# Kernel tuning notes

Hardware: AMD Instinct MI355X
Metric: run time of the kernel (lower is better)

## Reference

```python
import jax, jax.numpy as jnp
import numpy as np


def setup_inputs() -> dict:
    key = jax.random.key(0)
    k1, k2 = jax.random.split(key)
    TOKENS, IN, OUT = 32768, 1024, 1024
    x = jax.random.normal(k1, (TOKENS, IN), dtype=jnp.float32)
    # weight init: uniform(-1, 1) over [out_features, in_features]
    weight = jax.random.uniform(k2, (OUT, IN), dtype=jnp.float32, minval=-1.0, maxval=1.0)
    b = jnp.zeros((OUT,), dtype=jnp.float32)
    return {"x": x, "weight": weight, "b": b}


def reference(x, weight, b):
    # ternary quantization: sign() zeros out exact zeros; mask keeps nonzeros
    sign = jnp.sign(weight)
    mask = (weight != 0).astype(x.dtype)
    w_q = sign * mask  # [out, in], values in {-1, 0, 1}
    # F.linear: x @ w_q.T + b
    return jnp.einsum("ti,oi->to", x, w_q) + b
```

## Files before the change

kernel.cpp:

```cpp
#include <hip/hip_runtime.h>
#include <hip/hip_bf16.h>


typedef int   i32x4  __attribute__((ext_vector_type(4)));
typedef int   i32x16 __attribute__((ext_vector_type(16)));
typedef float f32x4  __attribute__((ext_vector_type(4)));

#define BM 128
#define BN 128
#define BK 64

__device__ __forceinline__ void async16(const void* gptr, void* lptr) {
    __builtin_amdgcn_global_load_lds(
        (const __attribute__((address_space(1))) unsigned int*)gptr,
        (__attribute__((address_space(3))) unsigned int*)lptr,
        16, 0, 0);
}

__device__ __forceinline__ int clamp127(int v) {
    v = v > 127 ? 127 : v;
    v = v < -127 ? -127 : v;
    return v;
}

__device__ __forceinline__ int pack4(int a, int b, int c, int d) {
    return (a & 255) | ((b & 255) << 8) | ((c & 255) << 16) | ((d & 255) << 24);
}

__device__ __forceinline__ int sgnb(float v) {
    return (v > 0.0f) ? 1 : ((v < 0.0f) ? -1 : 0);
}


__global__ __launch_bounds__(256)
void quant_pre(const float* __restrict__ x, const float* __restrict__ w,
               signed char* __restrict__ xq, signed char* __restrict__ wq,
               float* __restrict__ scales, int M, int K, long nw, int xblocks) {
    const int tid = threadIdx.x;

    if ((int)blockIdx.x >= xblocks) {
        long i = ((long)(blockIdx.x - xblocks) * 256 + tid) * 8;
        if (i + 8 > nw) return;
        const float4* p = (const float4*)(w + i);
        float4 a = p[0];
        float4 b = p[1];
        int lo = pack4(sgnb(a.x), sgnb(a.y), sgnb(a.z), sgnb(a.w));
        int hi = pack4(sgnb(b.x), sgnb(b.y), sgnb(b.z), sgnb(b.w));
        int2 v; v.x = lo; v.y = hi;
        *(int2*)(wq + i) = v;
        return;
    }

    const int wv   = tid >> 6;
    const int lane = tid & 63;
    const int row  = blockIdx.x * 4 + wv;
    if (row >= M) return;

    const float* xr = x + (long)row * K;
    const int chunks = K >> 8;
    float4 v[8];
    float m = 0.0f;
#pragma unroll
    for (int q = 0; q < 8; ++q) {
        if (q >= chunks) break;
        v[q] = *(const float4*)(xr + q * 256 + lane * 4);
        m = fmaxf(m, fmaxf(fmaxf(fabsf(v[q].x), fabsf(v[q].y)),
                           fmaxf(fabsf(v[q].z), fabsf(v[q].w))));
    }
#pragma unroll
    for (int off = 32; off > 0; off >>= 1)
        m = fmaxf(m, __shfl_xor(m, off, 64));

    const float inv = (m > 0.0f) ? (127.0f / m) : 0.0f;
    int* qr = (int*)(xq + (long)row * K);
#pragma unroll
    for (int q = 0; q < 8; ++q) {
        if (q >= chunks) break;
        int a = clamp127(__float2int_rn(v[q].x * inv));
        int b = clamp127(__float2int_rn(v[q].y * inv));
        int c = clamp127(__float2int_rn(v[q].z * inv));
        int d = clamp127(__float2int_rn(v[q].w * inv));
        qr[q * 64 + lane] = pack4(a, b, c, d);
    }
    if (lane == 0) scales[row] = m * (1.0f / 127.0f);
}


__global__ __launch_bounds__(256)
void gemm_i8(const signed char* __restrict__ A, const signed char* __restrict__ B,
             const float* __restrict__ scales, const float* __restrict__ bias,
             float* __restrict__ C, int M, int N, int K, int swz) {
    __shared__ __align__(16) signed char sA[2][64 * 128];
    __shared__ __align__(16) signed char sB[2][64 * 128];

    const int tid  = threadIdx.x;
    const int lane = tid & 63;
    const int wave = tid >> 6;

    const int gn = N / BN;
    int mt, nt;
    if (swz) {
        const int b    = blockIdx.x;
        const int xcd  = b & 7;
        const int rest = b >> 3;
        nt = rest % gn;
        mt = (rest / gn) * 8 + xcd;
    } else {
        nt = blockIdx.x % gn;
        mt = blockIdx.x / gn;
    }
    const int bm = mt * BM;
    const int bn = nt * BN;

    const int wrow = (wave >> 1) * 64;
    const int wcol = (wave & 1) * 64;
    const int l31  = lane & 31;
    const int ksel = lane >> 5;
    const int halfA = wave >> 1;
    const int halfB = wave & 1;

    const int s0 = tid, s1 = tid + 256;
    const int lr0 = s0 >> 3, lr1 = s1 >> 3;
    const int cc0 = (s0 & 7) ^ (lr0 & 7);
    const int cc1 = (s1 & 7) ^ (lr1 & 7);
    const long goA0 = (long)(bm + (cc0 >> 2) * 64 + lr0) * K + (cc0 & 3) * 16;
    const long goA1 = (long)(bm + (cc1 >> 2) * 64 + lr1) * K + (cc1 & 3) * 16;
    const long goB0 = (long)(bn + (cc0 >> 2) * 64 + lr0) * K + (cc0 & 3) * 16;
    const long goB1 = (long)(bn + (cc1 >> 2) * 64 + lr1) * K + (cc1 & 3) * 16;
    const int d0 = s0 * 16, d1 = s1 * 16;

#define STAGE(buf, k0)                                             \
    do {                                                           \
        async16(A + goA0 + (k0), (char*)sA[buf] + d0);             \
        async16(A + goA1 + (k0), (char*)sA[buf] + d1);             \
        async16(B + goB0 + (k0), (char*)sB[buf] + d0);             \
        async16(B + goB1 + (k0), (char*)sB[buf] + d1);             \
    } while (0)

    const int rsw = (l31 & 7) << 4;
    const int ccA0 = (halfA * 4 + 0 * 2 + ksel) << 4;
    const int ccA1 = (halfA * 4 + 1 * 2 + ksel) << 4;
    const int ccB0 = (halfB * 4 + 0 * 2 + ksel) << 4;
    const int ccB1 = (halfB * 4 + 1 * 2 + ksel) << 4;
    const int rA0 = l31 * 128;
    const int rA1 = (32 + l31) * 128;
    const int oA00 = rA0 + (ccA0 ^ rsw);
    const int oA01 = rA0 + (ccA1 ^ rsw);
    const int oA10 = rA1 + (ccA0 ^ rsw);
    const int oA11 = rA1 + (ccA1 ^ rsw);
    const int oB00 = rA0 + (ccB0 ^ rsw);
    const int oB01 = rA0 + (ccB1 ^ rsw);
    const int oB10 = rA1 + (ccB0 ^ rsw);
    const int oB11 = rA1 + (ccB1 ^ rsw);

    i32x16 acc00 = {}, acc01 = {}, acc10 = {}, acc11 = {};

#define COMPUTE(buf)                                                          \
    do {                                                                      \
        const signed char* a_ = sA[buf];                                      \
        const signed char* b_ = sB[buf];                                      \
        i32x4 a0 = *(const i32x4*)(a_ + oA00);                                \
        i32x4 a1 = *(const i32x4*)(a_ + oA10);                                \
        i32x4 b0 = *(const i32x4*)(b_ + oB00);                                \
        i32x4 b1 = *(const i32x4*)(b_ + oB10);                                \
        acc00 = __builtin_amdgcn_mfma_i32_32x32x32_i8(b0, a0, acc00, 0, 0, 0);\
        acc01 = __builtin_amdgcn_mfma_i32_32x32x32_i8(b1, a0, acc01, 0, 0, 0);\
        acc10 = __builtin_amdgcn_mfma_i32_32x32x32_i8(b0, a1, acc10, 0, 0, 0);\
        acc11 = __builtin_amdgcn_mfma_i32_32x32x32_i8(b1, a1, acc11, 0, 0, 0);\
        a0 = *(const i32x4*)(a_ + oA01);                                      \
        a1 = *(const i32x4*)(a_ + oA11);                                      \
        b0 = *(const i32x4*)(b_ + oB01);                                      \
        b1 = *(const i32x4*)(b_ + oB11);                                      \
        acc00 = __builtin_amdgcn_mfma_i32_32x32x32_i8(b0, a0, acc00, 0, 0, 0);\
        acc01 = __builtin_amdgcn_mfma_i32_32x32x32_i8(b1, a0, acc01, 0, 0, 0);\
        acc10 = __builtin_amdgcn_mfma_i32_32x32x32_i8(b0, a1, acc10, 0, 0, 0);\
        acc11 = __builtin_amdgcn_mfma_i32_32x32x32_i8(b1, a1, acc11, 0, 0, 0);\
    } while (0)

    const int NT = K / BK;
    STAGE(0, 0);
    __syncthreads();
    int k0 = 0;
    for (int t = 0; t < NT / 2 - 1; ++t) {
        STAGE(1, k0 + BK);
        COMPUTE(0);
        __syncthreads();
        STAGE(0, k0 + 2 * BK);
        COMPUTE(1);
        __syncthreads();
        k0 += 2 * BK;
    }
    STAGE(1, k0 + BK);
    COMPUTE(0);
    __syncthreads();
    COMPUTE(1);

#undef STAGE
#undef COMPUTE

#define STORE_FRAG(accv, i, j)                                          \
    do {                                                                \
        const int row = bm + wrow + (i) * 32 + l31;                     \
        const float sc = scales[row];                                   \
        float* cr = C + (long)row * N + bn + wcol + (j) * 32;           \
        _Pragma("unroll")                                               \
        for (int g = 0; g < 4; ++g) {                                   \
            const int n0 = g * 8 + ksel * 4;                            \
            const f32x4 bv = *(const f32x4*)&bias[bn + wcol + (j) * 32 + n0]; \
            f32x4 o;                                                    \
            o[0] = (float)(accv)[4 * g + 0] * sc + bv[0];               \
            o[1] = (float)(accv)[4 * g + 1] * sc + bv[1];               \
            o[2] = (float)(accv)[4 * g + 2] * sc + bv[2];               \
            o[3] = (float)(accv)[4 * g + 3] * sc + bv[3];               \
            *(f32x4*)&cr[n0] = o;                                       \
        }                                                               \
    } while (0)

    STORE_FRAG(acc00, 0, 0);
    STORE_FRAG(acc01, 0, 1);
    STORE_FRAG(acc10, 1, 0);
    STORE_FRAG(acc11, 1, 1);
#undef STORE_FRAG
}


__device__ __forceinline__ float signf(float v) {
    return (v > 0.0f) ? 1.0f : ((v < 0.0f) ? -1.0f : 0.0f);
}

__global__ void fallback_kernel(const float* __restrict__ x, const float* __restrict__ w,
                                const float* __restrict__ b, float* __restrict__ out,
                                int M, int N, int K) {
    long o = (long)blockIdx.x * blockDim.x + threadIdx.x;
    if (o >= (long)M * N) return;
    int t = (int)(o / N);
    int n = (int)(o % N);
    const float* xr = x + (long)t * K;
    const float* wr = w + (long)n * K;
    float s = 0.0f;
    for (int k = 0; k < K; ++k) s += xr[k] * signf(wr[k]);
    out[o] = s + b[n];
}


extern "C" void kernel_launch(void* const* d_in, const int* in_sizes, int n_in,
                              void* d_out, int out_size, void* d_ws, size_t ws_size,
                              hipStream_t stream) {
    const float* x = (const float*)d_in[0];
    const float* w = (const float*)d_in[1];
    const float* b = (const float*)d_in[2];
    float* out = (float*)d_out;

    const int N = in_sizes[2];
    const int K = in_sizes[1] / N;
    const int M = in_sizes[0] / K;

    const long nx = (long)M * K;
    const long nw = (long)N * K;
    const size_t need = (size_t)nx + (size_t)nw + (size_t)M * 4 + 64;

    const bool fast = (M % BM == 0) && (N % BN == 0) && (K % BK == 0) &&
                      (K % 256 == 0) && (K <= 2048) && (nw % 2048 == 0) &&
                      (ws_size >= need);

    if (!fast) {
        long total = (long)M * N;
        int blocks = (int)((total + 255) / 256);
        fallback_kernel<<<blocks, 256, 0, stream>>>(x, w, b, out, M, N, K);
        return;
    }

    signed char* xq = (signed char*)d_ws;
    signed char* wq = xq + nx;
    float* scales   = (float*)(wq + nw);

    const int xblocks = M / 4;
    const int wblocks = (int)(nw / 2048);
    quant_pre<<<xblocks + wblocks, 256, 0, stream>>>(x, w, xq, wq, scales, M, K, nw, xblocks);

    const int gm = M / BM, gn = N / BN;
    const int swz = (gm % 8 == 0) ? 1 : 0;
    gemm_i8<<<gm * gn, 256, 0, stream>>>(xq, wq, scales, b, out, M, N, K, swz);
}
```

Before: 289.3 us.

## Fuse quantization and int8 GEMM into one cooperative persistent kernel

Merges the activation/weight quantization pass and the int8 MFMA GEMM into a single cooperative launch. A grid-wide sync separates the two phases, and both phases loop over work in grid-stride persistent loops. Each wave now quantizes two rows, and K is limited to 1024. This removes a kernel launch and the gap between the two phases. In exchange it adds grid-sync cost, and it may hurt the XCD-aware tile mapping, since tiles are no longer tied one-to-one to block IDs.

```diff
diff --git a/kernel.cpp b/kernel.cpp
--- a/kernel.cpp
+++ b/kernel.cpp
@@ -1,6 +1,8 @@
 #include <hip/hip_runtime.h>
-#include <hip/hip_bf16.h>
-
+#include <hip/hip_cooperative_groups.h>
+
+
+namespace cg = cooperative_groups;
 
 typedef int   i32x4  __attribute__((ext_vector_type(4)));
 typedef int   i32x16 __attribute__((ext_vector_type(16)));
@@ -32,64 +34,79 @@
 }
 
 
-__global__ __launch_bounds__(256)
-void quant_pre(const float* __restrict__ x, const float* __restrict__ w,
-               signed char* __restrict__ xq, signed char* __restrict__ wq,
-               float* __restrict__ scales, int M, int K, long nw, int xblocks) {
+__device__ __forceinline__ void quant_group(
+    int g, int gx, const float* __restrict__ x, const float* __restrict__ w,
+    signed char* __restrict__ xq, signed char* __restrict__ wq,
+    float* __restrict__ scales, int M, int K, long nw) {
     const int tid = threadIdx.x;
 
-    if ((int)blockIdx.x >= xblocks) {
-        long i = ((long)(blockIdx.x - xblocks) * 256 + tid) * 8;
-        if (i + 8 > nw) return;
-        const float4* p = (const float4*)(w + i);
-        float4 a = p[0];
-        float4 b = p[1];
-        int lo = pack4(sgnb(a.x), sgnb(a.y), sgnb(a.z), sgnb(a.w));
-        int hi = pack4(sgnb(b.x), sgnb(b.y), sgnb(b.z), sgnb(b.w));
-        int2 v; v.x = lo; v.y = hi;
-        *(int2*)(wq + i) = v;
+    if (g >= gx) {
+        long i = ((long)(g - gx) * 256 + tid) * 8;
+        if (i + 8 <= nw) {
+            const float4* p = (const float4*)(w + i);
+            float4 a = p[0];
+            float4 b = p[1];
+            int lo = pack4(sgnb(a.x), sgnb(a.y), sgnb(a.z), sgnb(a.w));
+            int hi = pack4(sgnb(b.x), sgnb(b.y), sgnb(b.z), sgnb(b.w));
+            int2 v; v.x = lo; v.y = hi;
+            *(int2*)(wq + i) = v;
+        }
         return;
     }
 
     const int wv   = tid >> 6;
     const int lane = tid & 63;
-    const int row  = blockIdx.x * 4 + wv;
-    if (row >= M) return;
-
-    const float* xr = x + (long)row * K;
+    const int r0   = g * 8 + wv * 2;
+    if (r0 >= M) return;
+
+    const float* xa = x + (long)r0 * K;
+    const float* xb = xa + K;
     const int chunks = K >> 8;
-    float4 v[8];
-    float m = 0.0f;
+    float4 va[4], vb[4];
+    float ma = 0.0f, mb = 0.0f;
 #pragma unroll
-    for (int q = 0; q < 8; ++q) {
+    for (int q = 0; q < 4; ++q) {
         if (q >= chunks) break;
-        v[q] = *(const float4*)(xr + q * 256 + lane * 4);
-        m = fmaxf(m, fmaxf(fmaxf(fabsf(v[q].x), fabsf(v[q].y)),
-                           fmaxf(fabsf(v[q].z), fabsf(v[q].w))));
+        va[q] = *(const float4*)(xa + q * 256 + lane * 4);
+        vb[q] = *(const float4*)(xb + q * 256 + lane * 4);
+        ma = fmaxf(ma, fmaxf(fmaxf(fabsf(va[q].x), fabsf(va[q].y)),
+                             fmaxf(fabsf(va[q].z), fabsf(va[q].w))));
+        mb = fmaxf(mb, fmaxf(fmaxf(fabsf(vb[q].x), fabsf(vb[q].y)),
+                             fmaxf(fabsf(vb[q].z), fabsf(vb[q].w))));
     }
 #pragma unroll
-    for (int off = 32; off > 0; off >>= 1)
-        m = fmaxf(m, __shfl_xor(m, off, 64));
-
-    const float inv = (m > 0.0f) ? (127.0f / m) : 0.0f;
-    int* qr = (int*)(xq + (long)row * K);
+    for (int off = 32; off > 0; off >>= 1) {
+        ma = fmaxf(ma, __shfl_xor(ma, off, 64));
+        mb = fmaxf(mb, __shfl_xor(mb, off, 64));
+    }
+
+    const float ia = (ma > 0.0f) ? (127.0f / ma) : 0.0f;
+    const float ib = (mb > 0.0f) ? (127.0f / mb) : 0.0f;
+    int* qa = (int*)(xq + (long)r0 * K);
+    int* qb = (int*)(xq + (long)(r0 + 1) * K);
 #pragma unroll
-    for (int q = 0; q < 8; ++q) {
+    for (int q = 0; q < 4; ++q) {
         if (q >= chunks) break;
-        int a = clamp127(__float2int_rn(v[q].x * inv));
-        int b = clamp127(__float2int_rn(v[q].y * inv));
-        int c = clamp127(__float2int_rn(v[q].z * inv));
-        int d = clamp127(__float2int_rn(v[q].w * inv));
-        qr[q * 64 + lane] = pack4(a, b, c, d);
-    }
-    if (lane == 0) scales[row] = m * (1.0f / 127.0f);
-}
-
-
-__global__ __launch_bounds__(256)
-void gemm_i8(const signed char* __restrict__ A, const signed char* __restrict__ B,
-             const float* __restrict__ scales, const float* __restrict__ bias,
-             float* __restrict__ C, int M, int N, int K, int swz) {
+        qa[q * 64 + lane] = pack4(clamp127(__float2int_rn(va[q].x * ia)),
+                                  clamp127(__float2int_rn(va[q].y * ia)),
+                                  clamp127(__float2int_rn(va[q].z * ia)),
+                                  clamp127(__float2int_rn(va[q].w * ia)));
+        qb[q * 64 + lane] = pack4(clamp127(__float2int_rn(vb[q].x * ib)),
+                                  clamp127(__float2int_rn(vb[q].y * ib)),
+                                  clamp127(__float2int_rn(vb[q].z * ib)),
+                                  clamp127(__float2int_rn(vb[q].w * ib)));
+    }
+    if (lane == 0) {
+        scales[r0]     = ma * (1.0f / 127.0f);
+        scales[r0 + 1] = mb * (1.0f / 127.0f);
+    }
+}
+
+
+__device__ __forceinline__ void gemm_tile(
+    int t, const signed char* __restrict__ A, const signed char* __restrict__ B,
+    const float* __restrict__ scales, const float* __restrict__ bias,
+    float* __restrict__ C, int N, int K, int swz) {
     __shared__ __align__(16) signed char sA[2][64 * 128];
     __shared__ __align__(16) signed char sB[2][64 * 128];
 
@@ -100,14 +117,13 @@
     const int gn = N / BN;
     int mt, nt;
     if (swz) {
-        const int b    = blockIdx.x;
-        const int xcd  = b & 7;
-        const int rest = b >> 3;
+        const int xcd  = t & 7;
+        const int rest = t >> 3;
         nt = rest % gn;
         mt = (rest / gn) * 8 + xcd;
     } else {
-        nt = blockIdx.x % gn;
-        mt = blockIdx.x / gn;
+        nt = t % gn;
+        mt = t / gn;
     }
     const int bm = mt * BM;
     const int bn = nt * BN;
@@ -181,7 +197,7 @@
     STAGE(0, 0);
     __syncthreads();
     int k0 = 0;
-    for (int t = 0; t < NT / 2 - 1; ++t) {
+    for (int it = 0; it < NT / 2 - 1; ++it) {
         STAGE(1, k0 + BK);
         COMPUTE(0);
         __syncthreads();
@@ -224,6 +240,37 @@
 }
 
 
+__global__ __launch_bounds__(256)
+void fused_kernel(const float* __restrict__ x, const float* __restrict__ w,
+                  const float* __restrict__ bias,
+                  signed char* __restrict__ xq, signed char* __restrict__ wq,
+                  float* __restrict__ scales, float* __restrict__ C,
+                  int M, int N, int K, int swz, int gx, int gtot, int ntiles) {
+    const long nw = (long)N * K;
+    for (int g = blockIdx.x; g < gtot; g += gridDim.x)
+        quant_group(g, gx, x, w, xq, wq, scales, M, K, nw);
+    __threadfence();
+    cg::this_grid().sync();
+    for (int t = blockIdx.x; t < ntiles; t += gridDim.x)
+        gemm_tile(t, xq, wq, scales, bias, C, N, K, swz);
+}
+
+
+__global__ __launch_bounds__(256)
+void quant_pre(const float* __restrict__ x, const float* __restrict__ w,
+               signed char* __restrict__ xq, signed char* __restrict__ wq,
+               float* __restrict__ scales, int M, int K, long nw, int gx) {
+    quant_group(blockIdx.x, gx, x, w, xq, wq, scales, M, K, nw);
+}
+
+__global__ __launch_bounds__(256)
+void gemm_i8(const signed char* __restrict__ A, const signed char* __restrict__ B,
+             const float* __restrict__ scales, const float* __restrict__ bias,
+             float* __restrict__ C, int N, int K, int swz) {
+    gemm_tile(blockIdx.x, A, B, scales, bias, C, N, K, swz);
+}
+
+
 __device__ __forceinline__ float signf(float v) {
     return (v > 0.0f) ? 1.0f : ((v < 0.0f) ? -1.0f : 0.0f);
 }
@@ -260,7 +307,7 @@
     const size_t need = (size_t)nx + (size_t)nw + (size_t)M * 4 + 64;
 
     const bool fast = (M % BM == 0) && (N % BN == 0) && (K % BK == 0) &&
-                      (K % 256 == 0) && (K <= 2048) && (nw % 2048 == 0) &&
+                      (K % 256 == 0) && (K <= 1024) && (nw % 2048 == 0) &&
                       (ws_size >= need);
 
     if (!fast) {
@@ -274,11 +321,40 @@
     signed char* wq = xq + nx;
     float* scales   = (float*)(wq + nw);
 
-    const int xblocks = M / 4;
-    const int wblocks = (int)(nw / 2048);
-    quant_pre<<<xblocks + wblocks, 256, 0, stream>>>(x, w, xq, wq, scales, M, K, nw, xblocks);
-
+    const int gx     = M / 8;
+    const int wchunk = (int)(nw / 2048);
+    const int gtot   = gx + wchunk;
     const int gm = M / BM, gn = N / BN;
+    const int ntiles = gm * gn;
     const int swz = (gm % 8 == 0) ? 1 : 0;
-    gemm_i8<<<gm * gn, 256, 0, stream>>>(xq, wq, scales, b, out, M, N, K, swz);
-}
+
+    static int s_nb = -1, s_ncu = 0, s_coop = 0;
+    if (s_nb < 0) {
+        int dev = 0;
+        hipGetDevice(&dev);
+        hipDeviceGetAttribute(&s_ncu, hipDeviceAttributeMultiprocessorCount, dev);
+        hipDeviceGetAttribute(&s_coop, hipDeviceAttributeCooperativeLaunch, dev);
+        int nb = 0;
+        hipError_t oe = hipOccupancyMaxActiveBlocksPerMultiprocessor(
+            &nb, (const void*)fused_kernel, 256, 0);
+        s_nb = (oe == hipSuccess && nb >= 1) ? nb : 0;
+    }
+
+    bool done = false;
+    if (s_coop && s_nb >= 1 && s_ncu >= 8) {
+        int grid = s_nb * s_ncu;
+        if (grid > ntiles) grid = ntiles;
+        void* args[] = {(void*)&x, (void*)&w, (void*)&b,
+                        (void*)&xq, (void*)&wq, (void*)&scales, (void*)&out,
+                        (void*)&M, (void*)&N, (void*)&K, (void*)&swz,
+                        (void*)&gx, (void*)&gtot, (void*)&ntiles};
+        hipError_t e = hipLaunchCooperativeKernel(
+            (const void*)fused_kernel, dim3(grid), dim3(256), args, 0, stream);
+        done = (e == hipSuccess);
+    }
+
+    if (!done) {
+        quant_pre<<<gtot, 256, 0, stream>>>(x, w, xq, wq, scales, M, K, nw, gx);
+        gemm_i8<<<ntiles, 256, 0, stream>>>(xq, wq, scales, b, out, N, K, swz);
+    }
+}
```

Result: slower. 389.7 us (+34.7%).
